# Performance work log

Measured on AMD Instinct MI355X. Metric: run time of the kernel, lower is better.

The kernel has to match this reference:

```python
import jax, jax.numpy as jnp
import numpy as np

B, T, C, H, N = 4, 1024, 1024, 16, 64  # head_size N = 64 (hardcoded), H = C // N
FFN = 4 * C
EPS = 1e-5
HEAD_DIV = 8.0  # head_size_divisor


def setup_inputs():
    key = jax.random.key(0)
    ks = jax.random.split(key, 24)
    rn = lambda k, sh, s=0.02: jax.random.normal(k, sh, jnp.float32) * s
    ru = lambda k, sh: jax.random.uniform(k, sh, jnp.float32)
    return {
        "x": jax.random.normal(ks[0], (B, T, C), jnp.float32),
        "ln1_w": jnp.ones((C,), jnp.float32), "ln1_b": jnp.zeros((C,), jnp.float32),
        "ln2_w": jnp.ones((C,), jnp.float32), "ln2_b": jnp.zeros((C,), jnp.float32),
        "tm_mix_k": ru(ks[1], (C,)), "tm_mix_v": ru(ks[2], (C,)),
        "tm_mix_r": ru(ks[3], (C,)), "tm_mix_g": ru(ks[4], (C,)),
        "tm_decay": jax.random.uniform(ks[5], (H, N), jnp.float32, -6.0, -1.0),
        "tm_u": rn(ks[6], (H, N), 0.5),
        "Wr": rn(ks[7], (C, C)), "Wk": rn(ks[8], (C, C)), "Wv": rn(ks[9], (C, C)),
        "Wg": rn(ks[10], (C, C)), "Wo": rn(ks[11], (C, C)),
        "lnx_w": jnp.ones((C,), jnp.float32), "lnx_b": jnp.zeros((C,), jnp.float32),
        "cm_mix_k": ru(ks[12], (C,)), "cm_mix_r": ru(ks[13], (C,)),
        "cm_Wk": rn(ks[14], (FFN, C)), "cm_Wr": rn(ks[15], (C, C)), "cm_Wv": rn(ks[16], (C, FFN)),
    }


def _layernorm(x, w, b):
    m = x.mean(-1, keepdims=True)
    v = ((x - m) ** 2).mean(-1, keepdims=True)
    return (x - m) * jax.lax.rsqrt(v + EPS) * w + b


def _time_shift(x):
    # ZeroPad2d((0,0,1,-1)): shift sequence right by one, zero at t=0
    return jnp.concatenate([jnp.zeros_like(x[:, :1]), x[:, :-1]], axis=1)


def _wkv5(r, k, v, w, u):
    # r,k,v: [B,T,H,N]; w,u: [H,N]. Recurrent linear attention per head.
    ew = jnp.exp(-jnp.exp(w))  # decay in (0,1), [H,N]
    ewb = ew[None, :, :, None]  # decay along key dim i of state S[b,h,i,j]
    ub = u[None, :, :, None]

    def step(S, inp):
        rt, kt, vt = inp  # each [B,H,N]
        at = jnp.einsum('bhi,bhj->bhij', kt, vt)           # k_t outer v_t
        yt = jnp.einsum('bhi,bhij->bhj', rt, S + ub * at)   # r_t . (S + u*kv)
        S = ewb * S + at
        return S, yt

    xs = (jnp.swapaxes(r, 0, 1), jnp.swapaxes(k, 0, 1), jnp.swapaxes(v, 0, 1))  # [T,B,H,N]
    S0 = jnp.zeros((r.shape[0], r.shape[2], r.shape[3], v.shape[3]), r.dtype)
    _, ys = jax.lax.scan(step, S0, xs)
    return jnp.swapaxes(ys, 0, 1)  # [B,T,H,N]


def _groupnorm(x, w, b):
    # GroupNorm(H groups) over channel dim per token; x: [B,T,C]
    xh = x.reshape(B, T, H, N)
    m = xh.mean(-1, keepdims=True)
    v = ((xh - m) ** 2).mean(-1, keepdims=True)
    xn = (xh - m) * jax.lax.rsqrt(v + EPS)
    return (xn * w.reshape(H, N) + b.reshape(H, N)).reshape(B, T, C)


def _time_mix(x, tm_mix_k, tm_mix_v, tm_mix_r, tm_mix_g, tm_decay, tm_u,
              Wr, Wk, Wv, Wg, Wo, lnx_w, lnx_b):
    xx = _time_shift(x)
    xk = x * tm_mix_k + xx * (1 - tm_mix_k)
    xv = x * tm_mix_v + xx * (1 - tm_mix_v)
    xr = x * tm_mix_r + xx * (1 - tm_mix_r)
    xg = x * tm_mix_g + xx * (1 - tm_mix_g)
    r = (xr @ Wr.T).reshape(B, T, H, N)
    k = (xk @ Wk.T).reshape(B, T, H, N)
    v = (xv @ Wv.T).reshape(B, T, H, N)
    g = jax.nn.silu(xg @ Wg.T)
    y = _wkv5(r, k, v, tm_decay, tm_u).reshape(B, T, C)
    y = _groupnorm(y / HEAD_DIV, lnx_w, lnx_b)
    return (y * g) @ Wo.T


def _channel_mix(x, cm_mix_k, cm_mix_r, cm_Wk, cm_Wr, cm_Wv):
    xx = _time_shift(x)
    xk = x * cm_mix_k + xx * (1 - cm_mix_k)
    xr = x * cm_mix_r + xx * (1 - cm_mix_r)
    k = jnp.square(jax.nn.relu(xk @ cm_Wk.T))  # [B,T,4C]
    kv = k @ cm_Wv.T
    return jax.nn.sigmoid(xr @ cm_Wr.T) * kv


def reference(x, ln1_w, ln1_b, ln2_w, ln2_b,
              tm_mix_k, tm_mix_v, tm_mix_r, tm_mix_g, tm_decay, tm_u,
              Wr, Wk, Wv, Wg, Wo, lnx_w, lnx_b,
              cm_mix_k, cm_mix_r, cm_Wk, cm_Wr, cm_Wv):
    x = x + _time_mix(_layernorm(x, ln1_w, ln1_b), tm_mix_k, tm_mix_v, tm_mix_r,
                      tm_mix_g, tm_decay, tm_u, Wr, Wk, Wv, Wg, Wo, lnx_w, lnx_b)
    x = x + _channel_mix(_layernorm(x, ln2_w, ln2_b), cm_mix_k, cm_mix_r,
                         cm_Wk, cm_Wr, cm_Wv)
    return x
```

## Files before the change

kernel.cpp:

```cpp
#include <hip/hip_runtime.h>
#include <stdint.h>

typedef unsigned short u16;
typedef __attribute__((ext_vector_type(8))) short short8;
typedef __attribute__((ext_vector_type(4))) float f32x4;

#define BB 4
#define TT 1024
#define CC 1024
#define HH 16
#define NN 64
#define MM (BB*TT)
#define FFN_ 4096
#define PCH 16
#define LCH (TT/PCH)
static constexpr float EPS_ = 1e-5f;

__device__ __forceinline__ u16 f2bf(float f) {
    union { float f; uint32_t u; } x; x.f = f;
    uint32_t r = x.u + 0x7fff + ((x.u >> 16) & 1);
    return (u16)(r >> 16);
}
__device__ __forceinline__ float bf2f(u16 b) {
    union { uint32_t u; float f; } x; x.u = ((uint32_t)b) << 16; return x.f;
}

#define VMW8() asm volatile("s_waitcnt vmcnt(8)" ::: "memory")
#define VMW4() asm volatile("s_waitcnt vmcnt(4)" ::: "memory")
#define VMW0() asm volatile("s_waitcnt vmcnt(0)" ::: "memory")
#define BARRIER() do { asm volatile("" ::: "memory"); __builtin_amdgcn_s_barrier(); asm volatile("" ::: "memory"); } while (0)

__global__ __launch_bounds__(256) void lnz_kernel(const float* __restrict__ x,
    const float* __restrict__ w, const float* __restrict__ b, u16* __restrict__ z)
{
    int row = blockIdx.x;
    int tid = threadIdx.x;
    const float* xr = x + (size_t)row * CC;
    float4 v = ((const float4*)xr)[tid];
    float s  = v.x + v.y + v.z + v.w;
    float ss = v.x*v.x + v.y*v.y + v.z*v.z + v.w*v.w;
#pragma unroll
    for (int m = 1; m < 64; m <<= 1) { s += __shfl_xor(s, m); ss += __shfl_xor(ss, m); }
    __shared__ float as_[4], bs_[4];
    int wv = tid >> 6, ln = tid & 63;
    if (ln == 0) { as_[wv] = s; bs_[wv] = ss; }
    __syncthreads();
    s  = as_[0] + as_[1] + as_[2] + as_[3];
    ss = bs_[0] + bs_[1] + bs_[2] + bs_[3];
    float mean = s * (1.f / CC);
    float var  = ss * (1.f / CC) - mean * mean;
    float inv  = rsqrtf(var + EPS_);
    float4 w4 = ((const float4*)w)[tid];
    float4 b4 = ((const float4*)b)[tid];
    ushort4 o;
    o.x = f2bf((v.x - mean) * inv * w4.x + b4.x);
    o.y = f2bf((v.y - mean) * inv * w4.y + b4.y);
    o.z = f2bf((v.z - mean) * inv * w4.z + b4.z);
    o.w = f2bf((v.w - mean) * inv * w4.w + b4.w);
    int t = row & (TT - 1);
    *(ushort4*)(z + (size_t)row * 2048 + tid * 4) = o;
    if (t < TT - 1) *(ushort4*)(z + (size_t)(row + 1) * 2048 + 1024 + tid * 4) = o;
    if (t == 0) {
        ushort4 zz; zz.x = 0; zz.y = 0; zz.z = 0; zz.w = 0;
        *(ushort4*)(z + (size_t)row * 2048 + 1024 + tid * 4) = zz;
    }
}

__global__ __launch_bounds__(256) void mix2b_kernel(const u16* __restrict__ z2,
    const float* __restrict__ mk, const float* __restrict__ mr,
    u16* __restrict__ xk, u16* __restrict__ xr)
{
    int idx = blockIdx.x * 256 + threadIdx.x;
    int row = idx >> 8, c = (idx & 255) << 2;
    const u16* zr = z2 + (size_t)row * 2048;
    ushort4 zc = *(const ushort4*)(zr + c);
    ushort4 zp = *(const ushort4*)(zr + 1024 + c);
    float xc0 = bf2f(zc.x), xc1 = bf2f(zc.y), xc2 = bf2f(zc.z), xc3 = bf2f(zc.w);
    float xp0 = bf2f(zp.x), xp1 = bf2f(zp.y), xp2 = bf2f(zp.z), xp3 = bf2f(zp.w);
    float4 k4 = *(const float4*)(mk + c);
    float4 r4 = *(const float4*)(mr + c);
    ushort4 ok, orr;
    ok.x  = f2bf(xp0 + k4.x * (xc0 - xp0)); ok.y  = f2bf(xp1 + k4.y * (xc1 - xp1));
    ok.z  = f2bf(xp2 + k4.z * (xc2 - xp2)); ok.w  = f2bf(xp3 + k4.w * (xc3 - xp3));
    orr.x = f2bf(xp0 + r4.x * (xc0 - xp0)); orr.y = f2bf(xp1 + r4.y * (xc1 - xp1));
    orr.z = f2bf(xp2 + r4.z * (xc2 - xp2)); orr.w = f2bf(xp3 + r4.w * (xc3 - xp3));
    size_t f = (size_t)row * 1024 + c;
    *(ushort4*)(xk + f) = ok;
    *(ushort4*)(xr + f) = orr;
}

__global__ __launch_bounds__(256) void convW4_kernel(
    const float* __restrict__ Wr, const float* __restrict__ Wk,
    const float* __restrict__ Wv, const float* __restrict__ Wg,
    const float* __restrict__ mr, const float* __restrict__ mk,
    const float* __restrict__ mv, const float* __restrict__ mg,
    u16* __restrict__ W4p)
{
    int idx = blockIdx.x * 256 + threadIdx.x;
    int n = idx >> 8, c = (idx & 255) << 2;
    int sel = n >> 10, nr = n & 1023;
    const float* W = sel == 0 ? Wr : sel == 1 ? Wk : sel == 2 ? Wv : Wg;
    const float* mx = sel == 0 ? mr : sel == 1 ? mk : sel == 2 ? mv : mg;
    float4 w4 = *(const float4*)(W + (size_t)nr * 1024 + c);
    float4 m4 = *(const float4*)(mx + c);
    ushort4 a, bq;
    a.x  = f2bf(w4.x * m4.x); a.y  = f2bf(w4.y * m4.y);
    a.z  = f2bf(w4.z * m4.z); a.w  = f2bf(w4.w * m4.w);
    bq.x = f2bf(w4.x * (1.f - m4.x)); bq.y = f2bf(w4.y * (1.f - m4.y));
    bq.z = f2bf(w4.z * (1.f - m4.z)); bq.w = f2bf(w4.w * (1.f - m4.w));
    *(ushort4*)(W4p + (size_t)n * 2048 + c) = a;
    *(ushort4*)(W4p + (size_t)n * 2048 + 1024 + c) = bq;
}

struct ConvArgs {
    const float* src[8];
    u16* dst[8];
    int start4[8];
};
__global__ __launch_bounds__(256) void conv_kernel(ConvArgs a, int total4)
{
    int i4 = blockIdx.x * 256 + threadIdx.x;
    if (i4 >= total4) return;
    int s = 0;
#pragma unroll
    for (int j = 1; j < 8; ++j) if (i4 >= a.start4[j]) s = j;
    int l4 = i4 - a.start4[s];
    float4 v = ((const float4*)a.src[s])[l4];
    ushort4 o; o.x = f2bf(v.x); o.y = f2bf(v.y); o.z = f2bf(v.z); o.w = f2bf(v.w);
    ((ushort4*)a.dst[s])[l4] = o;
}

__device__ __forceinline__ void stage_tile(const u16* gbase, int rbase, int ldk,
                                           int kcol, u16* ldsbase, int tid)
{
#pragma unroll
    for (int rd = 0; rd < 2; ++rd) {
        int row = rd * 128 + (tid >> 2);
        int slog = (tid & 3) ^ ((row >> 1) & 3);
        const u16* src = gbase + (size_t)(rbase + row) * ldk + kcol + (slog << 3);
        u16* dst = ldsbase + row * 32 + ((tid & 3) << 3);
        __builtin_amdgcn_global_load_lds(
            (const __attribute__((address_space(1))) uint32_t*)(const void*)src,
            (__attribute__((address_space(3))) uint32_t*)(void*)dst, 16, 0, 0);
    }
}

template<int EPI>
__global__ __launch_bounds__(512, 2) void gemm8(
    const u16* __restrict__ A, const u16* __restrict__ Bw,
    float* __restrict__ Cf, u16* __restrict__ Cbf,
    int Mdim, int Ndim, int Kdim, int kLen)
{
    __shared__ u16 As[4 * 8192];
    __shared__ u16 Bs[4 * 8192];
    int tid = threadIdx.x;
    int wid = tid >> 6, lane = tid & 63;
    int wm = wid >> 2, wn = wid & 3;
    int f = lane & 15, g = lane >> 4;

    int nwg = gridDim.x * gridDim.y;
    int bid = blockIdx.y * gridDim.x + blockIdx.x;
    int qq = nwg >> 3, r8 = nwg & 7;
    int xcd = bid & 7, lid = bid >> 3;
    int swz = (xcd < r8 ? xcd * (qq + 1) : r8 * (qq + 1) + (xcd - r8) * qq) + lid;
    int bx = swz % gridDim.x, by = swz / gridDim.x;
    int rowBase = by * 256, colBase = bx * 256;
    int kOff = blockIdx.z * kLen;
    int NT = kLen >> 5;
    if (EPI == 7) Cf += (size_t)blockIdx.z * Mdim * Ndim;

    f32x4 acc[8][4] = {};

    stage_tile(A,  rowBase, Kdim, kOff,      As, tid);
    stage_tile(Bw, colBase, Kdim, kOff,      Bs, tid);
    if (NT > 1) {
        stage_tile(A,  rowBase, Kdim, kOff + 32, As + 8192, tid);
        stage_tile(Bw, colBase, Kdim, kOff + 32, Bs + 8192, tid);
    }
    if (NT > 2) {
        stage_tile(A,  rowBase, Kdim, kOff + 64, As + 2 * 8192, tid);
        stage_tile(Bw, colBase, Kdim, kOff + 64, Bs + 2 * 8192, tid);
    }

    for (int t = 0; t < NT; ++t) {
        if (t < NT - 2) { VMW8(); } else if (t == NT - 2) { VMW4(); } else { VMW0(); }
        BARRIER();
        const u16* Asl = As + (t & 3) * 8192;
        const u16* Bsl = Bs + (t & 3) * 8192;
        short8 bfr[4], afr[4];
#pragma unroll
        for (int n = 0; n < 4; ++n) {
            int row = wn * 64 + n * 16 + f;
            bfr[n] = *(const short8*)(Bsl + row * 32 + ((g ^ ((row >> 1) & 3)) << 3));
        }
#pragma unroll
        for (int m = 0; m < 4; ++m) {
            int row = wm * 128 + m * 16 + f;
            afr[m] = *(const short8*)(Asl + row * 32 + ((g ^ ((row >> 1) & 3)) << 3));
        }
        if (t + 3 < NT)
            stage_tile(A, rowBase, Kdim, kOff + (t + 3) * 32, As + ((t + 3) & 3) * 8192, tid);
        __builtin_amdgcn_s_setprio(1);
#pragma unroll
        for (int m = 0; m < 4; ++m)
#pragma unroll
            for (int n = 0; n < 4; ++n)
                acc[m][n] = __builtin_amdgcn_mfma_f32_16x16x32_bf16(afr[m], bfr[n], acc[m][n], 0, 0, 0);
        __builtin_amdgcn_s_setprio(0);
#pragma unroll
        for (int m = 0; m < 4; ++m) {
            int row = wm * 128 + 64 + m * 16 + f;
            afr[m] = *(const short8*)(Asl + row * 32 + ((g ^ ((row >> 1) & 3)) << 3));
        }
        if (t + 3 < NT)
            stage_tile(Bw, colBase, Kdim, kOff + (t + 3) * 32, Bs + ((t + 3) & 3) * 8192, tid);
        __builtin_amdgcn_s_setprio(1);
#pragma unroll
        for (int m = 0; m < 4; ++m)
#pragma unroll
            for (int n = 0; n < 4; ++n)
                acc[4 + m][n] = __builtin_amdgcn_mfma_f32_16x16x32_bf16(afr[m], bfr[n], acc[4 + m][n], 0, 0, 0);
        __builtin_amdgcn_s_setprio(0);
    }

    int r0 = rowBase + wm * 128, c0 = colBase + wn * 64;
    bool dsilu = (EPI == 6) && (colBase >= 3072);
#pragma unroll
    for (int am = 0; am < 8; ++am) {
#pragma unroll
        for (int n = 0; n < 4; ++n) {
#pragma unroll
            for (int rg = 0; rg < 4; ++rg) {
                int gr = r0 + am * 16 + (lane >> 4) * 4 + rg;
                int gc = c0 + n * 16 + (lane & 15);
                size_t idx = (size_t)gr * Ndim + gc;
                float v = acc[am][n][rg];
                if (EPI == 3) { float rr = v > 0.f ? v : 0.f; Cbf[idx] = f2bf(rr * rr); }
                else if (EPI == 6) Cf[idx] = dsilu ? v / (1.f + __expf(-v)) : v;
                else Cf[idx] = v;
            }
        }
    }
}

template<int EPI>
__global__ __launch_bounds__(256) void gemm_bt(
    const u16* __restrict__ A, const u16* __restrict__ Bw,
    float* __restrict__ Cf, u16* __restrict__ Cbf,
    const float* __restrict__ aux1, const float* __restrict__ aux2,
    int Mdim, int Ndim, int Kdim)
{
    __shared__ u16 As[128 * 32];
    __shared__ u16 Bs[128 * 32];
    int tid = threadIdx.x;
    int w = tid >> 6, lane = tid & 63;
    int bx = blockIdx.x, by = blockIdx.y;
    int rowBase = by * 128, colBase = bx * 128;
    int wr = w >> 1, wc = w & 1;
    int fr = lane & 15, fk = (lane >> 4) * 8;

    f32x4 acc[4][4] = {};

    int nK = Kdim >> 5;
    for (int kt = 0; kt < nK; ++kt) {
        int k0 = kt << 5;
#pragma unroll
        for (int q = 0; q < 2; ++q) {
            int c = w * 128 + q * 64 + lane;
            const u16* ga = A + (size_t)(rowBase + (c >> 2)) * Kdim + k0 + ((c & 3) << 3);
            __builtin_amdgcn_global_load_lds(
                (const __attribute__((address_space(1))) uint32_t*)(const void*)ga,
                (__attribute__((address_space(3))) uint32_t*)(void*)(As + (size_t)(w * 128 + q * 64) * 8),
                16, 0, 0);
            const u16* gb = Bw + (size_t)(colBase + (c >> 2)) * Kdim + k0 + ((c & 3) << 3);
            __builtin_amdgcn_global_load_lds(
                (const __attribute__((address_space(1))) uint32_t*)(const void*)gb,
                (__attribute__((address_space(3))) uint32_t*)(void*)(Bs + (size_t)(w * 128 + q * 64) * 8),
                16, 0, 0);
        }
        __syncthreads();
        short8 af[4], bf[4];
#pragma unroll
        for (int m = 0; m < 4; ++m)
            af[m] = *(const short8*)&As[(wr * 64 + m * 16 + fr) * 32 + fk];
#pragma unroll
        for (int n = 0; n < 4; ++n)
            bf[n] = *(const short8*)&Bs[(wc * 64 + n * 16 + fr) * 32 + fk];
#pragma unroll
        for (int m = 0; m < 4; ++m)
#pragma unroll
            for (int n = 0; n < 4; ++n)
                acc[m][n] = __builtin_amdgcn_mfma_f32_16x16x32_bf16(af[m], bf[n], acc[m][n], 0, 0, 0);
        __syncthreads();
    }

    int r0 = rowBase + wr * 64, c0 = colBase + wc * 64;
#pragma unroll
    for (int m = 0; m < 4; ++m) {
#pragma unroll
        for (int n = 0; n < 4; ++n) {
#pragma unroll
            for (int rg = 0; rg < 4; ++rg) {
                int gr = r0 + m * 16 + (lane >> 4) * 4 + rg;
                int gc = c0 + n * 16 + (lane & 15);
                size_t idx = (size_t)gr * Ndim + gc;
                float v = acc[m][n][rg];
                if (EPI == 2) Cf[idx] = aux1[idx] + v;
                else if (EPI == 4) Cf[idx] = 1.f / (1.f + __expf(-v));
                else Cf[idx] = v;
            }
        }
    }
}

__device__ __forceinline__ size_t sidx(int b, int h, int c, int i, int j) {
    return ((((size_t)b * HH + h) * PCH + c) * NN + i) * NN + j;
}

__global__ __launch_bounds__(64) void wkv_p1(
    const float* __restrict__ k, const float* __restrict__ v,
    const float* __restrict__ decay, float* __restrict__ Sloc, int ld)
{
    int blk = blockIdx.x;
    int c  = blk & (PCH - 1);
    int jb = (blk >> 4) & 3;
    int h  = (blk >> 6) & (HH - 1);
    int b  = blk >> 10;
    int lane = threadIdx.x;
    int jj = lane & 15, g = lane >> 4;
    __shared__ float kbufS[64];
    float S[16], ew[16];
#pragma unroll
    for (int ii = 0; ii < 16; ++ii) {
        int i = g * 16 + ii;
        S[ii] = 0.f;
        ew[ii] = expf(-expf(decay[h * NN + i]));
    }
    const size_t base = ((size_t)b * TT + c * LCH) * ld + h * NN;
    const float* kb = k + base;
    const float* vb = v + base + jb * 16;

    for (int t = 0; t < LCH; ++t) {
        size_t off = (size_t)t * ld;
        float kv_ = kb[off + lane];
        float vv  = vb[off + jj];
        kbufS[lane] = kv_;
        __syncthreads();
        float4 kq[4];
#pragma unroll
        for (int q = 0; q < 4; ++q) kq[q] = ((const float4*)kbufS)[g * 4 + q];
        const float* kf = (const float*)kq;
#pragma unroll
        for (int ii = 0; ii < 16; ++ii)
            S[ii] = fmaf(ew[ii], S[ii], kf[ii] * vv);
        __syncthreads();
    }
#pragma unroll
    for (int ii = 0; ii < 16; ++ii)
        Sloc[sidx(b, h, c, g * 16 + ii, jb * 16 + jj)] = S[ii];
}

__global__ __launch_bounds__(64) void wkv_p2(
    const float* __restrict__ decay,
    const float* __restrict__ Sloc, float* __restrict__ Sst)
{
    int blk = blockIdx.x;
    int jb = blk & 3;
    int h  = (blk >> 2) & (HH - 1);
    int b  = blk >> 6;
    int lane = threadIdx.x;
    int jj = lane & 15, g = lane >> 4;
    float Srun[16], ewL[16];
#pragma unroll
    for (int ii = 0; ii < 16; ++ii) {
        int i = g * 16 + ii;
        Srun[ii] = 0.f;
        ewL[ii] = expf(-expf(decay[h * NN + i]) * (float)LCH);
    }
    int j = jb * 16 + jj;
    for (int c = 0; c < PCH; ++c) {
#pragma unroll
        for (int ii = 0; ii < 16; ++ii) {
            size_t id = sidx(b, h, c, g * 16 + ii, j);
            Sst[id] = Srun[ii];
            Srun[ii] = fmaf(ewL[ii], Srun[ii], Sloc[id]);
        }
    }
}

__global__ __launch_bounds__(64) void wkv_p3(
    const float* __restrict__ r, const float* __restrict__ k, const float* __restrict__ v,
    const float* __restrict__ decay, const float* __restrict__ u,
    const float* __restrict__ Sst, float* __restrict__ y, int ld)
{
    int blk = blockIdx.x;
    int c  = blk & (PCH - 1);
    int jb = (blk >> 4) & 3;
    int h  = (blk >> 6) & (HH - 1);
    int b  = blk >> 10;
    int lane = threadIdx.x;
    int jj = lane & 15, g = lane >> 4;
    __shared__ float rkbuf[128];
    float S[16], uu[16], ew[16];
#pragma unroll
    for (int ii = 0; ii < 16; ++ii) {
        int i = g * 16 + ii;
        S[ii] = Sst[sidx(b, h, c, i, jb * 16 + jj)];
        ew[ii] = expf(-expf(decay[h * NN + i]));
        uu[ii] = u[h * NN + i];
    }
    const size_t base = ((size_t)b * TT + c * LCH) * ld + h * NN;
    const float* rb = r + base;
    const float* kb = k + base;
    const float* vb = v + base + jb * 16;
    float* yb = y + (((size_t)b * TT + c * LCH)) * CC + h * NN + jb * 16;

    for (int t = 0; t < LCH; ++t) {
        size_t off = (size_t)t * ld;
        float rv  = rb[off + lane];
        float kv_ = kb[off + lane];
        float vv  = vb[off + jj];
        rkbuf[2 * lane]     = rv;
        rkbuf[2 * lane + 1] = kv_;
        __syncthreads();
        float acc = 0.f;
        const float2* rk2 = (const float2*)rkbuf;
#pragma unroll
        for (int ii = 0; ii < 16; ++ii) {
            float2 p = rk2[g * 16 + ii];
            float kvv = p.y * vv;
            float t1 = fmaf(uu[ii], kvv, S[ii]);
            acc = fmaf(p.x, t1, acc);
            S[ii] = fmaf(ew[ii], S[ii], kvv);
        }
        acc += __shfl_xor(acc, 16);
        acc += __shfl_xor(acc, 32);
        if (g == 0) yb[(size_t)t * CC + jj] = acc;
        __syncthreads();
    }
}

__global__ __launch_bounds__(256) void gn_kernel(const float* __restrict__ y,
    const float* __restrict__ gsil, const float* __restrict__ w, const float* __restrict__ b,
    u16* __restrict__ og)
{
    int row = blockIdx.x;
    int tid = threadIdx.x;
    int head = tid >> 4, q = tid & 15;
    int cb = head * NN + q * 4;
    size_t base = (size_t)row * CC + cb;
    float4 v = *(const float4*)(y + base);
    v.x *= 0.125f; v.y *= 0.125f; v.z *= 0.125f; v.w *= 0.125f;
    float s  = v.x + v.y + v.z + v.w;
    float ss = v.x*v.x + v.y*v.y + v.z*v.z + v.w*v.w;
#pragma unroll
    for (int m = 1; m < 16; m <<= 1) { s += __shfl_xor(s, m); ss += __shfl_xor(ss, m); }
    float mean = s * (1.f / NN);
    float var  = ss * (1.f / NN) - mean * mean;
    float inv  = rsqrtf(var + EPS_);
    float4 w4 = *(const float4*)(w + cb);
    float4 b4 = *(const float4*)(b + cb);
    float4 g4 = *(const float4*)(gsil + (size_t)row * 4096 + cb);
    ushort4 o;
    o.x = f2bf(((v.x - mean) * inv * w4.x + b4.x) * g4.x);
    o.y = f2bf(((v.y - mean) * inv * w4.y + b4.y) * g4.y);
    o.z = f2bf(((v.z - mean) * inv * w4.z + b4.z) * g4.z);
    o.w = f2bf(((v.w - mean) * inv * w4.w + b4.w) * g4.w);
    *(ushort4*)(og + base) = o;
}

__global__ __launch_bounds__(256) void reduce_cmv(const float* __restrict__ p,
    const float* __restrict__ x1, const float* __restrict__ sr, float* __restrict__ out)
{
    size_t i = ((size_t)blockIdx.x * 256 + threadIdx.x) * 4;
    const size_t stride = (size_t)MM * 1024;
    float4 a0 = *(const float4*)(p + i);
    float4 a1 = *(const float4*)(p + stride + i);
    float4 a2 = *(const float4*)(p + 2 * stride + i);
    float4 a3 = *(const float4*)(p + 3 * stride + i);
    float4 xv = *(const float4*)(x1 + i);
    float4 sv = *(const float4*)(sr + i);
    float4 o;
    o.x = xv.x + sv.x * (a0.x + a1.x + a2.x + a3.x);
    o.y = xv.y + sv.y * (a0.y + a1.y + a2.y + a3.y);
    o.z = xv.z + sv.z * (a0.z + a1.z + a2.z + a3.z);
    o.w = xv.w + sv.w * (a0.w + a1.w + a2.w + a3.w);
    *(float4*)(out + i) = o;
}

extern "C" void kernel_launch(void* const* d_in, const int* in_sizes, int n_in,
                              void* d_out, int out_size, void* d_ws, size_t ws_size,
                              hipStream_t stream)
{
    const float* x       = (const float*)d_in[0];
    const float* ln1_w   = (const float*)d_in[1];
    const float* ln1_b   = (const float*)d_in[2];
    const float* ln2_w   = (const float*)d_in[3];
    const float* ln2_b   = (const float*)d_in[4];
    const float* tm_mix_k= (const float*)d_in[5];
    const float* tm_mix_v= (const float*)d_in[6];
    const float* tm_mix_r= (const float*)d_in[7];
    const float* tm_mix_g= (const float*)d_in[8];
    const float* tm_decay= (const float*)d_in[9];
    const float* tm_u    = (const float*)d_in[10];
    const float* Wr      = (const float*)d_in[11];
    const float* Wk      = (const float*)d_in[12];
    const float* Wv      = (const float*)d_in[13];
    const float* Wg      = (const float*)d_in[14];
    const float* Wo      = (const float*)d_in[15];
    const float* lnx_w   = (const float*)d_in[16];
    const float* lnx_b   = (const float*)d_in[17];
    const float* cm_mix_k= (const float*)d_in[18];
    const float* cm_mix_r= (const float*)d_in[19];
    const float* cm_Wk   = (const float*)d_in[20];
    const float* cm_Wr   = (const float*)d_in[21];
    const float* cm_Wv   = (const float*)d_in[22];

    char* ws = (char*)d_ws;
    auto MB = [](size_t m) { return m * 1024ull * 1024ull; };
    u16*   z      = (u16*)(ws + 0);
    float* rkvg   = (float*)(ws + MB(16));
    float* partials = (float*)(ws + MB(16));
    float* ybuf   = (float*)(ws + MB(80));
    float* sr     = (float*)(ws + MB(80));
    u16*   og     = (u16*)(ws + MB(96));
    u16*   xk     = (u16*)(ws + MB(96));
    u16*   xr     = (u16*)(ws + MB(104));
    float* Sloc   = (float*)(ws + MB(112));
    float* x1     = (float*)(ws + MB(112));
    u16*   W4p    = (u16*)(ws + MB(128));
    float* Sst    = (float*)(ws + MB(128));
    u16*   kbuf2  = (u16*)(ws + MB(128));
    u16*   Wo_b   = (u16*)(ws + MB(160));
    u16*   cmWk_b = (u16*)(ws + MB(162));
    u16*   cmWr_b = (u16*)(ws + MB(170));
    u16*   cmWv_b = (u16*)(ws + MB(172));

    convW4_kernel<<<4096, 256, 0, stream>>>(Wr, Wk, Wv, Wg,
        tm_mix_r, tm_mix_k, tm_mix_v, tm_mix_g, W4p);
    ConvArgs ca;
    ca.src[0] = Wo;    ca.dst[0] = Wo_b;
    ca.src[1] = cm_Wk; ca.dst[1] = cmWk_b;
    ca.src[2] = cm_Wr; ca.dst[2] = cmWr_b;
    ca.src[3] = cm_Wv; ca.dst[3] = cmWv_b;
    int q = (CC * CC) / 4;
    ca.start4[0] = 0; ca.start4[1] = q; ca.start4[2] = 5 * q; ca.start4[3] = 6 * q;
    for (int i = 4; i < 8; ++i) { ca.src[i] = Wo; ca.dst[i] = Wo_b; ca.start4[i] = 0x7FFFFFFF; }
    int total4 = 10 * q;
    conv_kernel<<<(total4 + 255) / 256, 256, 0, stream>>>(ca, total4);

    lnz_kernel<<<MM, 256, 0, stream>>>(x, ln1_w, ln1_b, z);

    gemm8<6><<<dim3(16, 16, 1), 512, 0, stream>>>(z, W4p, rkvg, nullptr, MM, 4096, 2048, 2048);

    wkv_p1<<<BB * HH * 4 * PCH, 64, 0, stream>>>(rkvg + 1024, rkvg + 2048, tm_decay, Sloc, 4096);
    wkv_p2<<<BB * HH * 4, 64, 0, stream>>>(tm_decay, Sloc, Sst);
    wkv_p3<<<BB * HH * 4 * PCH, 64, 0, stream>>>(rkvg, rkvg + 1024, rkvg + 2048,
                                                 tm_decay, tm_u, Sst, ybuf, 4096);

    gn_kernel<<<MM, 256, 0, stream>>>(ybuf, rkvg + 3072, lnx_w, lnx_b, og);

    dim3 g1(CC / 128, MM / 128);
    gemm_bt<2><<<g1, 256, 0, stream>>>(og, Wo_b, x1, nullptr, x, nullptr, MM, CC, CC);

    lnz_kernel<<<MM, 256, 0, stream>>>(x1, ln2_w, ln2_b, z);
    mix2b_kernel<<<4096, 256, 0, stream>>>(z, cm_mix_k, cm_mix_r, xk, xr);

    gemm8<3><<<dim3(16, 16, 1), 512, 0, stream>>>(xk, cmWk_b, nullptr, kbuf2, MM, 4096, 1024, 1024);
    gemm_bt<4><<<g1, 256, 0, stream>>>(xr, cmWr_b, sr, nullptr, nullptr, nullptr, MM, CC, CC);

    gemm8<7><<<dim3(4, 16, 4), 512, 0, stream>>>(kbuf2, cmWv_b, partials, nullptr, MM, 1024, 4096, 1024);

    reduce_cmv<<<4096, 256, 0, stream>>>(partials, x1, sr, (float*)d_out);
}
```

Baseline: 503.5 us.

## Restructure GEMM LDS pipeline into 8-slot half-tile ring with deeper prefetch

Replaces the separate 4-deep A and B LDS buffers with a unified 8-slot ring of half-tiles and processes two 32-wide K steps per loop iteration. A and B tiles are staged six half-tiles ahead, and extra barriers are added after each stage issue. The aim is finer-grained overlap of global-to-LDS loads with MFMA work. The cost is more barriers per iteration, and the wait counts (VMW8/VMW4/VMW0) must still match the number of outstanding loads. The code also now assumes kLen is a multiple of 64.

```diff
diff --git a/kernel.cpp b/kernel.cpp
--- a/kernel.cpp
+++ b/kernel.cpp
@@ -151,8 +151,7 @@
     float* __restrict__ Cf, u16* __restrict__ Cbf,
     int Mdim, int Ndim, int Kdim, int kLen)
 {
-    __shared__ u16 As[4 * 8192];
-    __shared__ u16 Bs[4 * 8192];
+    __shared__ u16 ring[8][8192];
     int tid = threadIdx.x;
     int wid = tid >> 6, lane = tid & 63;
     int wm = wid >> 2, wn = wid & 3;
@@ -166,40 +165,40 @@
     int bx = swz % gridDim.x, by = swz / gridDim.x;
     int rowBase = by * 256, colBase = bx * 256;
     int kOff = blockIdx.z * kLen;
-    int NT = kLen >> 5;
+    int NT = kLen >> 6;
+    int HMAX = NT << 2;
     if (EPI == 7) Cf += (size_t)blockIdx.z * Mdim * Ndim;
 
     f32x4 acc[8][4] = {};
 
-    stage_tile(A,  rowBase, Kdim, kOff,      As, tid);
-    stage_tile(Bw, colBase, Kdim, kOff,      Bs, tid);
-    if (NT > 1) {
-        stage_tile(A,  rowBase, Kdim, kOff + 32, As + 8192, tid);
-        stage_tile(Bw, colBase, Kdim, kOff + 32, Bs + 8192, tid);
-    }
-    if (NT > 2) {
-        stage_tile(A,  rowBase, Kdim, kOff + 64, As + 2 * 8192, tid);
-        stage_tile(Bw, colBase, Kdim, kOff + 64, Bs + 2 * 8192, tid);
-    }
+    auto STAGE = [&](int h) {
+        if (h >= HMAX) return;
+        int kc = kOff + ((h >> 2) << 6) + (((h >> 1) & 1) << 5);
+        if ((h & 1) == 0) stage_tile(A,  rowBase, Kdim, kc, ring[h & 7], tid);
+        else              stage_tile(Bw, colBase, Kdim, kc, ring[h & 7], tid);
+    };
+
+    for (int h = 0; h < 6; ++h) STAGE(h);
 
     for (int t = 0; t < NT; ++t) {
-        if (t < NT - 2) { VMW8(); } else if (t == NT - 2) { VMW4(); } else { VMW0(); }
+        int hb = t << 2;
+        if (t < NT - 1) { VMW8(); } else { VMW4(); }
         BARRIER();
-        const u16* Asl = As + (t & 3) * 8192;
-        const u16* Bsl = Bs + (t & 3) * 8192;
+        const u16* Aslot = ring[(hb + 0) & 7];
+        const u16* Bslot = ring[(hb + 1) & 7];
         short8 bfr[4], afr[4];
 #pragma unroll
         for (int n = 0; n < 4; ++n) {
             int row = wn * 64 + n * 16 + f;
-            bfr[n] = *(const short8*)(Bsl + row * 32 + ((g ^ ((row >> 1) & 3)) << 3));
+            bfr[n] = *(const short8*)(Bslot + row * 32 + ((g ^ ((row >> 1) & 3)) << 3));
         }
 #pragma unroll
         for (int m = 0; m < 4; ++m) {
             int row = wm * 128 + m * 16 + f;
-            afr[m] = *(const short8*)(Asl + row * 32 + ((g ^ ((row >> 1) & 3)) << 3));
-        }
-        if (t + 3 < NT)
-            stage_tile(A, rowBase, Kdim, kOff + (t + 3) * 32, As + ((t + 3) & 3) * 8192, tid);
+            afr[m] = *(const short8*)(Aslot + row * 32 + ((g ^ ((row >> 1) & 3)) << 3));
+        }
+        STAGE(hb + 6);
+        BARRIER();
         __builtin_amdgcn_s_setprio(1);
 #pragma unroll
         for (int m = 0; m < 4; ++m)
@@ -210,10 +209,47 @@
 #pragma unroll
         for (int m = 0; m < 4; ++m) {
             int row = wm * 128 + 64 + m * 16 + f;
-            afr[m] = *(const short8*)(Asl + row * 32 + ((g ^ ((row >> 1) & 3)) << 3));
-        }
-        if (t + 3 < NT)
-            stage_tile(Bw, colBase, Kdim, kOff + (t + 3) * 32, Bs + ((t + 3) & 3) * 8192, tid);
+            afr[m] = *(const short8*)(Aslot + row * 32 + ((g ^ ((row >> 1) & 3)) << 3));
+        }
+        STAGE(hb + 7);
+        BARRIER();
+        __builtin_amdgcn_s_setprio(1);
+#pragma unroll
+        for (int m = 0; m < 4; ++m)
+#pragma unroll
+            for (int n = 0; n < 4; ++n)
+                acc[4 + m][n] = __builtin_amdgcn_mfma_f32_16x16x32_bf16(afr[m], bfr[n], acc[4 + m][n], 0, 0, 0);
+        __builtin_amdgcn_s_setprio(0);
+        if (t < NT - 1) { VMW8(); } else { VMW0(); }
+        BARRIER();
+        Aslot = ring[(hb + 2) & 7];
+        Bslot = ring[(hb + 3) & 7];
+#pragma unroll
+        for (int n = 0; n < 4; ++n) {
+            int row = wn * 64 + n * 16 + f;
+            bfr[n] = *(const short8*)(Bslot + row * 32 + ((g ^ ((row >> 1) & 3)) << 3));
+        }
+#pragma unroll
+        for (int m = 0; m < 4; ++m) {
+            int row = wm * 128 + m * 16 + f;
+            afr[m] = *(const short8*)(Aslot + row * 32 + ((g ^ ((row >> 1) & 3)) << 3));
+        }
+        STAGE(hb + 8);
+        BARRIER();
+        __builtin_amdgcn_s_setprio(1);
+#pragma unroll
+        for (int m = 0; m < 4; ++m)
+#pragma unroll
+            for (int n = 0; n < 4; ++n)
+                acc[m][n] = __builtin_amdgcn_mfma_f32_16x16x32_bf16(afr[m], bfr[n], acc[m][n], 0, 0, 0);
+        __builtin_amdgcn_s_setprio(0);
+#pragma unroll
+        for (int m = 0; m < 4; ++m) {
+            int row = wm * 128 + 64 + m * 16 + f;
+            afr[m] = *(const short8*)(Aslot + row * 32 + ((g ^ ((row >> 1) & 3)) << 3));
+        }
+        STAGE(hb + 9);
+        BARRIER();
         __builtin_amdgcn_s_setprio(1);
 #pragma unroll
         for (int m = 0; m < 4; ++m)
```

Result: faster. 489.5 us (-2.8%).

## Pipeline 128x128 GEMMs with 4-stage LDS ring, XCD swizzle, fuse prep kernels

Applied to the files above, without the earlier changes.

Replaces the single-buffered gemm_bt, which synchronised twice per K step, with gemmr. gemmr keeps a 4-slot LDS ring with three tiles in flight, uses XOR-swizzled LDS addressing, remaps blocks across the XCDs for cache locality, and raises MFMA priority. The goal is to hide global load latency in the Wo and cm_Wr GEMMs. The two weight-conversion kernels are also merged into one launch. The larger LDS footprint (64KB) may limit occupancy, and the 2-blocks-per-CU launch bound assumes it fits.

```diff
diff --git a/kernel.cpp b/kernel.cpp
--- a/kernel.cpp
+++ b/kernel.cpp
@@ -89,45 +89,43 @@
     *(ushort4*)(xr + f) = orr;
 }
 
-__global__ __launch_bounds__(256) void convW4_kernel(
-    const float* __restrict__ Wr, const float* __restrict__ Wk,
-    const float* __restrict__ Wv, const float* __restrict__ Wg,
-    const float* __restrict__ mr, const float* __restrict__ mk,
-    const float* __restrict__ mv, const float* __restrict__ mg,
-    u16* __restrict__ W4p)
-{
-    int idx = blockIdx.x * 256 + threadIdx.x;
-    int n = idx >> 8, c = (idx & 255) << 2;
-    int sel = n >> 10, nr = n & 1023;
-    const float* W = sel == 0 ? Wr : sel == 1 ? Wk : sel == 2 ? Wv : Wg;
-    const float* mx = sel == 0 ? mr : sel == 1 ? mk : sel == 2 ? mv : mg;
-    float4 w4 = *(const float4*)(W + (size_t)nr * 1024 + c);
-    float4 m4 = *(const float4*)(mx + c);
-    ushort4 a, bq;
-    a.x  = f2bf(w4.x * m4.x); a.y  = f2bf(w4.y * m4.y);
-    a.z  = f2bf(w4.z * m4.z); a.w  = f2bf(w4.w * m4.w);
-    bq.x = f2bf(w4.x * (1.f - m4.x)); bq.y = f2bf(w4.y * (1.f - m4.y));
-    bq.z = f2bf(w4.z * (1.f - m4.z)); bq.w = f2bf(w4.w * (1.f - m4.w));
-    *(ushort4*)(W4p + (size_t)n * 2048 + c) = a;
-    *(ushort4*)(W4p + (size_t)n * 2048 + 1024 + c) = bq;
-}
-
-struct ConvArgs {
-    const float* src[8];
-    u16* dst[8];
-    int start4[8];
+struct PrepArgs {
+    const float *Wr, *Wk, *Wv, *Wg, *mr, *mk, *mv, *mg;
+    u16* W4p;
+    const float* csrc[4];
+    u16* cdst[4];
+    int cstart4[4];
+    int ctotal4;
 };
-__global__ __launch_bounds__(256) void conv_kernel(ConvArgs a, int total4)
-{
-    int i4 = blockIdx.x * 256 + threadIdx.x;
-    if (i4 >= total4) return;
-    int s = 0;
-#pragma unroll
-    for (int j = 1; j < 8; ++j) if (i4 >= a.start4[j]) s = j;
-    int l4 = i4 - a.start4[s];
-    float4 v = ((const float4*)a.src[s])[l4];
-    ushort4 o; o.x = f2bf(v.x); o.y = f2bf(v.y); o.z = f2bf(v.z); o.w = f2bf(v.w);
-    ((ushort4*)a.dst[s])[l4] = o;
+__global__ __launch_bounds__(256) void prep_kernel(PrepArgs a)
+{
+    int bid = blockIdx.x;
+    if (bid < 4096) {
+        int idx = bid * 256 + threadIdx.x;
+        int n = idx >> 8, c = (idx & 255) << 2;
+        int sel = n >> 10, nr = n & 1023;
+        const float* W = sel == 0 ? a.Wr : sel == 1 ? a.Wk : sel == 2 ? a.Wv : a.Wg;
+        const float* mx = sel == 0 ? a.mr : sel == 1 ? a.mk : sel == 2 ? a.mv : a.mg;
+        float4 w4 = *(const float4*)(W + (size_t)nr * 1024 + c);
+        float4 m4 = *(const float4*)(mx + c);
+        ushort4 p, q4;
+        p.x  = f2bf(w4.x * m4.x); p.y  = f2bf(w4.y * m4.y);
+        p.z  = f2bf(w4.z * m4.z); p.w  = f2bf(w4.w * m4.w);
+        q4.x = f2bf(w4.x * (1.f - m4.x)); q4.y = f2bf(w4.y * (1.f - m4.y));
+        q4.z = f2bf(w4.z * (1.f - m4.z)); q4.w = f2bf(w4.w * (1.f - m4.w));
+        *(ushort4*)(a.W4p + (size_t)n * 2048 + c) = p;
+        *(ushort4*)(a.W4p + (size_t)n * 2048 + 1024 + c) = q4;
+    } else {
+        int i4 = (bid - 4096) * 256 + threadIdx.x;
+        if (i4 >= a.ctotal4) return;
+        int s = 0;
+#pragma unroll
+        for (int j = 1; j < 4; ++j) if (i4 >= a.cstart4[j]) s = j;
+        int l4 = i4 - a.cstart4[s];
+        float4 v = ((const float4*)a.csrc[s])[l4];
+        ushort4 o; o.x = f2bf(v.x); o.y = f2bf(v.y); o.z = f2bf(v.z); o.w = f2bf(v.w);
+        ((ushort4*)a.cdst[s])[l4] = o;
+    }
 }
 
 __device__ __forceinline__ void stage_tile(const u16* gbase, int rbase, int ldk,
@@ -243,58 +241,83 @@
     }
 }
 
+__device__ __forceinline__ void stage_tile128(const u16* gbase, int rbase, int ldk,
+                                              int kcol, u16* ldsbase, int tid)
+{
+#pragma unroll
+    for (int rd = 0; rd < 2; ++rd) {
+        int row = rd * 64 + (tid >> 2);
+        int slog = (tid & 3) ^ ((row >> 1) & 3);
+        const u16* src = gbase + (size_t)(rbase + row) * ldk + kcol + (slog << 3);
+        u16* dst = ldsbase + row * 32 + ((tid & 3) << 3);
+        __builtin_amdgcn_global_load_lds(
+            (const __attribute__((address_space(1))) uint32_t*)(const void*)src,
+            (__attribute__((address_space(3))) uint32_t*)(void*)dst, 16, 0, 0);
+    }
+}
+
 template<int EPI>
-__global__ __launch_bounds__(256) void gemm_bt(
+__global__ __launch_bounds__(256, 2) void gemmr(
     const u16* __restrict__ A, const u16* __restrict__ Bw,
-    float* __restrict__ Cf, u16* __restrict__ Cbf,
-    const float* __restrict__ aux1, const float* __restrict__ aux2,
+    float* __restrict__ Cf,
+    const float* __restrict__ aux1,
     int Mdim, int Ndim, int Kdim)
 {
-    __shared__ u16 As[128 * 32];
-    __shared__ u16 Bs[128 * 32];
+    __shared__ u16 As[4 * 4096];
+    __shared__ u16 Bs[4 * 4096];
     int tid = threadIdx.x;
-    int w = tid >> 6, lane = tid & 63;
-    int bx = blockIdx.x, by = blockIdx.y;
+    int wid = tid >> 6, lane = tid & 63;
+    int wm = wid >> 1, wn = wid & 1;
+    int f = lane & 15, g = lane >> 4;
+
+    int nwg = gridDim.x * gridDim.y;
+    int bid = blockIdx.y * gridDim.x + blockIdx.x;
+    int qq = nwg >> 3, r8 = nwg & 7;
+    int xcd = bid & 7, lid = bid >> 3;
+    int swz = (xcd < r8 ? xcd * (qq + 1) : r8 * (qq + 1) + (xcd - r8) * qq) + lid;
+    int bx = swz % gridDim.x, by = swz / gridDim.x;
     int rowBase = by * 128, colBase = bx * 128;
-    int wr = w >> 1, wc = w & 1;
-    int fr = lane & 15, fk = (lane >> 4) * 8;
+    int NT = Kdim >> 5;
 
     f32x4 acc[4][4] = {};
 
-    int nK = Kdim >> 5;
-    for (int kt = 0; kt < nK; ++kt) {
-        int k0 = kt << 5;
-#pragma unroll
-        for (int q = 0; q < 2; ++q) {
-            int c = w * 128 + q * 64 + lane;
-            const u16* ga = A + (size_t)(rowBase + (c >> 2)) * Kdim + k0 + ((c & 3) << 3);
-            __builtin_amdgcn_global_load_lds(
-                (const __attribute__((address_space(1))) uint32_t*)(const void*)ga,
-                (__attribute__((address_space(3))) uint32_t*)(void*)(As + (size_t)(w * 128 + q * 64) * 8),
-                16, 0, 0);
-            const u16* gb = Bw + (size_t)(colBase + (c >> 2)) * Kdim + k0 + ((c & 3) << 3);
-            __builtin_amdgcn_global_load_lds(
-                (const __attribute__((address_space(1))) uint32_t*)(const void*)gb,
-                (__attribute__((address_space(3))) uint32_t*)(void*)(Bs + (size_t)(w * 128 + q * 64) * 8),
-                16, 0, 0);
-        }
-        __syncthreads();
-        short8 af[4], bf[4];
+    stage_tile128(A,  rowBase, Kdim, 0,  As, tid);
+    stage_tile128(Bw, colBase, Kdim, 0,  Bs, tid);
+    stage_tile128(A,  rowBase, Kdim, 32, As + 4096, tid);
+    stage_tile128(Bw, colBase, Kdim, 32, Bs + 4096, tid);
+    stage_tile128(A,  rowBase, Kdim, 64, As + 2 * 4096, tid);
+    stage_tile128(Bw, colBase, Kdim, 64, Bs + 2 * 4096, tid);
+
+    for (int t = 0; t < NT; ++t) {
+        if (t < NT - 2) { VMW8(); } else if (t == NT - 2) { VMW4(); } else { VMW0(); }
+        BARRIER();
+        const u16* Asl = As + (t & 3) * 4096;
+        const u16* Bsl = Bs + (t & 3) * 4096;
+        short8 bfr[4], afr[4];
+#pragma unroll
+        for (int n = 0; n < 4; ++n) {
+            int row = wn * 64 + n * 16 + f;
+            bfr[n] = *(const short8*)(Bsl + row * 32 + ((g ^ ((row >> 1) & 3)) << 3));
+        }
+#pragma unroll
+        for (int m = 0; m < 4; ++m) {
+            int row = wm * 64 + m * 16 + f;
+            afr[m] = *(const short8*)(Asl + row * 32 + ((g ^ ((row >> 1) & 3)) << 3));
+        }
+        if (t + 3 < NT) {
+            stage_tile128(A,  rowBase, Kdim, (t + 3) * 32, As + ((t + 3) & 3) * 4096, tid);
+            stage_tile128(Bw, colBase, Kdim, (t + 3) * 32, Bs + ((t + 3) & 3) * 4096, tid);
+        }
+        __builtin_amdgcn_s_setprio(1);
 #pragma unroll
         for (int m = 0; m < 4; ++m)
-            af[m] = *(const short8*)&As[(wr * 64 + m * 16 + fr) * 32 + fk];
-#pragma unroll
-        for (int n = 0; n < 4; ++n)
-            bf[n] = *(const short8*)&Bs[(wc * 64 + n * 16 + fr) * 32 + fk];
-#pragma unroll
-        for (int m = 0; m < 4; ++m)
 #pragma unroll
             for (int n = 0; n < 4; ++n)
-                acc[m][n] = __builtin_amdgcn_mfma_f32_16x16x32_bf16(af[m], bf[n], acc[m][n], 0, 0, 0);
-        __syncthreads();
-    }
-
-    int r0 = rowBase + wr * 64, c0 = colBase + wc * 64;
+                acc[m][n] = __builtin_amdgcn_mfma_f32_16x16x32_bf16(afr[m], bfr[n], acc[m][n], 0, 0, 0);
+        __builtin_amdgcn_s_setprio(0);
+    }
+
+    int r0 = rowBase + wm * 64, c0 = colBase + wn * 64;
 #pragma unroll
     for (int m = 0; m < 4; ++m) {
 #pragma unroll
@@ -306,8 +329,7 @@
                 size_t idx = (size_t)gr * Ndim + gc;
                 float v = acc[m][n][rg];
                 if (EPI == 2) Cf[idx] = aux1[idx] + v;
-                else if (EPI == 4) Cf[idx] = 1.f / (1.f + __expf(-v));
-                else Cf[idx] = v;
+                else Cf[idx] = 1.f / (1.f + __expf(-v));
             }
         }
     }
@@ -536,18 +558,18 @@
     u16*   cmWr_b = (u16*)(ws + MB(170));
     u16*   cmWv_b = (u16*)(ws + MB(172));
 
-    convW4_kernel<<<4096, 256, 0, stream>>>(Wr, Wk, Wv, Wg,
-        tm_mix_r, tm_mix_k, tm_mix_v, tm_mix_g, W4p);
-    ConvArgs ca;
-    ca.src[0] = Wo;    ca.dst[0] = Wo_b;
-    ca.src[1] = cm_Wk; ca.dst[1] = cmWk_b;
-    ca.src[2] = cm_Wr; ca.dst[2] = cmWr_b;
-    ca.src[3] = cm_Wv; ca.dst[3] = cmWv_b;
+    PrepArgs pa;
+    pa.Wr = Wr; pa.Wk = Wk; pa.Wv = Wv; pa.Wg = Wg;
+    pa.mr = tm_mix_r; pa.mk = tm_mix_k; pa.mv = tm_mix_v; pa.mg = tm_mix_g;
+    pa.W4p = W4p;
+    pa.csrc[0] = Wo;    pa.cdst[0] = Wo_b;
+    pa.csrc[1] = cm_Wk; pa.cdst[1] = cmWk_b;
+    pa.csrc[2] = cm_Wr; pa.cdst[2] = cmWr_b;
+    pa.csrc[3] = cm_Wv; pa.cdst[3] = cmWv_b;
     int q = (CC * CC) / 4;
-    ca.start4[0] = 0; ca.start4[1] = q; ca.start4[2] = 5 * q; ca.start4[3] = 6 * q;
-    for (int i = 4; i < 8; ++i) { ca.src[i] = Wo; ca.dst[i] = Wo_b; ca.start4[i] = 0x7FFFFFFF; }
-    int total4 = 10 * q;
-    conv_kernel<<<(total4 + 255) / 256, 256, 0, stream>>>(ca, total4);
+    pa.cstart4[0] = 0; pa.cstart4[1] = q; pa.cstart4[2] = 5 * q; pa.cstart4[3] = 6 * q;
+    pa.ctotal4 = 10 * q;
+    prep_kernel<<<4096 + (10 * q + 255) / 256, 256, 0, stream>>>(pa);
 
     lnz_kernel<<<MM, 256, 0, stream>>>(x, ln1_w, ln1_b, z);
 
@@ -560,14 +582,14 @@
 
     gn_kernel<<<MM, 256, 0, stream>>>(ybuf, rkvg + 3072, lnx_w, lnx_b, og);
 
-    dim3 g1(CC / 128, MM / 128);
-    gemm_bt<2><<<g1, 256, 0, stream>>>(og, Wo_b, x1, nullptr, x, nullptr, MM, CC, CC);
+    dim3 gr1(CC / 128, MM / 128);
+    gemmr<2><<<gr1, 256, 0, stream>>>(og, Wo_b, x1, x, MM, CC, CC);
 
     lnz_kernel<<<MM, 256, 0, stream>>>(x1, ln2_w, ln2_b, z);
     mix2b_kernel<<<4096, 256, 0, stream>>>(z, cm_mix_k, cm_mix_r, xk, xr);
 
     gemm8<3><<<dim3(16, 16, 1), 512, 0, stream>>>(xk, cmWk_b, nullptr, kbuf2, MM, 4096, 1024, 1024);
-    gemm_bt<4><<<g1, 256, 0, stream>>>(xr, cmWr_b, sr, nullptr, nullptr, nullptr, MM, CC, CC);
+    gemmr<4><<<gr1, 256, 0, stream>>>(xr, cmWr_b, sr, nullptr, MM, CC, CC);
 
     gemm8<7><<<dim3(4, 16, 4), 512, 0, stream>>>(kbuf2, cmWv_b, partials, nullptr, MM, 1024, 4096, 1024);
 
```

Result: faster. 465.9 us (-7.5%).
